# Optimization experiments

Measured on AMD Instinct MI355X. Metric: run time of the kernel, lower is better.

Reference implementation:

```python
import jax, jax.numpy as jnp
import numpy as np

C = 19          # EEG channels
NP = C * C      # 361 channel pairs
D = 256         # UNIFIED_FEATURE_DIM
H = 8           # num_heads
HD = D // H     # head dim


def _build_mask():
    # rel[p, q] = True iff key-pair q shares a channel with query-pair p
    idx = np.arange(NP)
    ci, cj = idx // C, idx % C
    rel = ((ci[:, None] == ci[None, :]) | (ci[:, None] == cj[None, :]) |
           (cj[:, None] == ci[None, :]) | (cj[:, None] == cj[None, :]))
    return jnp.asarray(rel.reshape(C, C, NP))  # (channel_i, j, key_pair)

MASK = _build_mask()


def setup_inputs() -> dict:
    key = jax.random.key(0)
    ks = jax.random.split(key, 6)
    s = 0.05
    return {
        "x": jax.random.normal(ks[0], (32, NP, D), jnp.float32),
        # 19 stacked nn.MultiheadAttention modules: in_proj (3D, D) = [Wq; Wk; Wv]
        "w_in": jax.random.normal(ks[1], (C, 3 * D, D), jnp.float32) * s,
        "b_in": jnp.zeros((C, 3 * D), jnp.float32),
        "w_out": jax.random.normal(ks[2], (C, D, D), jnp.float32) * s,
        "b_out": jnp.zeros((C, D), jnp.float32),
        # fusion: nn.Linear(D, D)
        "w_fuse": jax.random.normal(ks[3], (D, D), jnp.float32) * s,
        "b_fuse": jnp.zeros((D,), jnp.float32),
    }


def reference(x, w_in, b_in, w_out, b_out, w_fuse, b_fuse):
    # x: (B, 361, D). Pair p=(i,j) at index i*19+j uses attention module i,
    # query = x[:, p], keys/values = pairs sharing channel i or j (mask).
    B = x.shape[0]
    wq, wk, wv = w_in[:, :D], w_in[:, D:2 * D], w_in[:, 2 * D:]
    bq, bk, bv = b_in[:, :D], b_in[:, D:2 * D], b_in[:, 2 * D:]

    # Per-channel K/V projections over all 361 pairs: (C, B, NP, D)
    K = jnp.einsum('bnd,ced->cbne', x, wk) + bk[:, None, None, :]
    V = jnp.einsum('bnd,ced->cbne', x, wv) + bv[:, None, None, :]
    # Queries grouped by first channel i: x reshaped to (B, C, C, D)
    xq = x.reshape(B, C, C, D)
    Q = jnp.einsum('bcjd,ced->cbje', xq, wq) + bq[:, None, None, :]  # (C,B,C,D)

    Qh = Q.reshape(C, B, C, H, HD)
    Kh = K.reshape(C, B, NP, H, HD)
    Vh = V.reshape(C, B, NP, H, HD)

    scale = 1.0 / jnp.sqrt(jnp.asarray(HD, x.dtype))
    scores = jnp.einsum('cbqhe,cbkhe->cbhqk', Qh, Kh) * scale  # (C,B,H,C,NP)
    scores = jnp.where(MASK[:, None, None, :, :], scores, -jnp.inf)
    attn = jax.nn.softmax(scores, axis=-1)

    out = jnp.einsum('cbhqk,cbkhe->cbqhe', attn, Vh).reshape(C, B, C, D)
    out = jnp.einsum('cbqd,ced->cbqe', out, w_out) + b_out[:, None, None, :]
    out = out.transpose(1, 0, 2, 3).reshape(B, NP, D)  # back to (B, 361, D)

    # fusion ('linear') + residual
    return out @ w_fuse.T + b_fuse + x
```

## Files before the change

kernel.cpp:

```cpp
#include <hip/hip_runtime.h>

#define CC 19
#define NPOS 361
#define NPAD 384
#define DIM 256
#define TKEY 32
#define NTILES 12

#define LDS_BYTES 69632

using bf16x8 = __attribute__((ext_vector_type(8))) short;
using f16x4  = __attribute__((ext_vector_type(4))) _Float16;
using floatx4 = __attribute__((ext_vector_type(4))) float;
using uintx2 = __attribute__((ext_vector_type(2))) unsigned int;

__device__ __forceinline__ unsigned short f2bf(float f) {
  unsigned u = __builtin_bit_cast(unsigned, f);
  u += 0x7fffu + ((u >> 16) & 1u);
  return (unsigned short)(u >> 16);
}

__device__ __forceinline__ f16x4 pack4h(float a, float b, float c2, float d) {
  const auto h01 = __builtin_amdgcn_cvt_pkrtz(a, b);
  const auto h23 = __builtin_amdgcn_cvt_pkrtz(c2, d);
  uintx2 uv = {__builtin_bit_cast(unsigned, h01), __builtin_bit_cast(unsigned, h23)};
  return __builtin_bit_cast(f16x4, uv);
}

__global__ void conv_all_kernel(const float* __restrict__ x,
                                const float* __restrict__ w_in,
                                const float* __restrict__ w_out,
                                const float* __restrict__ w_fuse,
                                unsigned short* __restrict__ ws) {
  const int j = blockIdx.x * 256 + threadIdx.x;
  float4 v = make_float4(0.f, 0.f, 0.f, 0.f);
  unsigned short* dst;
  if (j < 786432) {
    const int row = j >> 6;
    const int off = (j & 63) << 2;
    const int b = row / NPAD;
    const int r = row - b * NPAD;
    if (r < NPOS) v = *(const float4*)&x[(b * NPOS + r) * DIM + off];
    dst = &ws[row * DIM + off];
  } else if (j < 1720320) {
    const int k = j - 786432;
    v = *(const float4*)&w_in[k << 2];
    dst = &ws[3145728 + (k << 2)];
  } else if (j < 2031616) {
    const int k = j - 1720320;
    v = *(const float4*)&w_out[k << 2];
    dst = &ws[6881280 + (k << 2)];
  } else {
    const int k = j - 2031616;
    v = *(const float4*)&w_fuse[k << 2];
    dst = &ws[8126464 + (k << 2)];
  }
  ushort4 o;
  o.x = f2bf(v.x); o.y = f2bf(v.y); o.z = f2bf(v.z); o.w = f2bf(v.w);
  *(ushort4*)dst = o;
}

__launch_bounds__(256, 2)
__global__ void attn_kernel(const float* __restrict__ b_in,
                            const unsigned short* __restrict__ xbf,
                            const unsigned short* __restrict__ wibf,
                            float* __restrict__ out) {
  const int bid = blockIdx.x;
  const int xcd = bid & 7;
  const int slot = bid >> 3;
  const int c = slot >> 3;
  const int p = ((slot & 7) << 3) | xcd;
  const int b = p >> 1;
  const int hb = p & 1;

  const int tid = threadIdx.x;
  const int w = tid >> 6;
  const int lane = tid & 63;
  const int quad = lane >> 4;
  const int l16 = lane & 15;
  const int eh = (hb * 4 + w) * 32;

  extern __shared__ char smem[];
  unsigned short* sx = (unsigned short*)smem;
  unsigned* msk = (unsigned*)(smem + 67584);
  float* sL = (float*)(smem + 69120);

  const float scale = 0.25503486f;
  const floatx4 fzero = {0.f, 0.f, 0.f, 0.f};

  f16x4 qf[2][2];
  {
    bf16x8 wq[2][8];
#pragma unroll
    for (int m4 = 0; m4 < 2; ++m4)
#pragma unroll
      for (int k = 0; k < 8; ++k)
        wq[m4][k] = *(const bf16x8*)&wibf[(c * 768 + eh + m4 * 16 + l16) * DIM + k * 32 + quad * 8];
    float bq[2][4];
#pragma unroll
    for (int m4 = 0; m4 < 2; ++m4) {
      const float4 bv4 = *(const float4*)&b_in[c * 768 + eh + m4 * 16 + quad * 4];
      bq[m4][0] = bv4.x; bq[m4][1] = bv4.y; bq[m4][2] = bv4.z; bq[m4][3] = bv4.w;
    }
#pragma unroll
    for (int mt = 0; mt < 2; ++mt) {
      const int xrow = b * NPAD + c * CC + mt * 16 + l16;
      bf16x8 xq[8];
#pragma unroll
      for (int k = 0; k < 8; ++k)
        xq[k] = *(const bf16x8*)&xbf[xrow * DIM + k * 32 + quad * 8];
#pragma unroll
      for (int m4 = 0; m4 < 2; ++m4) {
        floatx4 acc = fzero;
#pragma unroll
        for (int k = 0; k < 8; ++k)
          acc = __builtin_amdgcn_mfma_f32_16x16x32_bf16(wq[m4][k], xq[k], acc, 0, 0, 0);
        qf[mt][m4] = pack4h((acc[0] + bq[m4][0]) * scale, (acc[1] + bq[m4][1]) * scale,
                            (acc[2] + bq[m4][2]) * scale, (acc[3] + bq[m4][3]) * scale);
      }
    }
  }

  bf16x8 wk[2][8], wv[2][8];
#pragma unroll
  for (int m4 = 0; m4 < 2; ++m4)
#pragma unroll
    for (int k = 0; k < 8; ++k) {
      wk[m4][k] =
          *(const bf16x8*)&wibf[(c * 768 + 256 + eh + m4 * 16 + l16) * DIM + k * 32 + quad * 8];
      wv[m4][k] =
          *(const bf16x8*)&wibf[(c * 768 + 512 + eh + m4 * 16 + l16) * DIM + k * 32 + quad * 8];
    }
  float bV[2];
#pragma unroll
  for (int ne = 0; ne < 2; ++ne) bV[ne] = b_in[c * 768 + 512 + eh + ne * 16 + l16];

  for (int e2 = tid; e2 < 384; e2 += 256) {
    const int q = e2 / 12;
    const int wd = e2 - q * 12;
    unsigned m = 0u;
    for (int i = 0; i < 32; ++i) {
      const int kabs = wd * 32 + i;
      const unsigned ki = ((unsigned)kabs * 110377u) >> 21;
      const unsigned kj = (unsigned)kabs - ki * 19u;
      if (kabs < NPOS && (ki == (unsigned)c || kj == (unsigned)c ||
                          ki == (unsigned)q || kj == (unsigned)q))
        m |= (1u << i);
    }
    msk[e2] = m;
  }

#pragma unroll
  for (int u = 0; u < 2; ++u)
#pragma unroll
    for (int it = 0; it < 4; ++it) {
      const int cc2 = tid + it * 256;
      const int row = cc2 >> 5;
      const int col = (cc2 & 31) * 8;
      *(bf16x8*)&sx[u * 8448 + row * 264 + col] =
          *(const bf16x8*)&xbf[(b * NPAD + u * TKEY + row) * DIM + col];
    }

  floatx4 o_acc[2][2];
  float lsum[2] = {0.f, 0.f};
#pragma unroll
  for (int mt = 0; mt < 2; ++mt)
#pragma unroll
    for (int ne = 0; ne < 2; ++ne) o_acc[mt][ne] = fzero;

  __syncthreads();

  for (int s6 = 0; s6 < 6; ++s6) {
    const int tb = s6 * 2;
    if (s6 < 5) {
#pragma unroll
      for (int u = 0; u < 2; ++u) {
        const int t = tb + 2 + u;
        unsigned short* bxn = sx + (t & 3) * 8448;
#pragma unroll
        for (int it = 0; it < 4; ++it) {
          const int cc2 = tid + it * 256;
          const int row = cc2 >> 5;
          const int col = (cc2 & 31) * 8;
          *(bf16x8*)&bxn[row * 264 + col] =
              *(const bf16x8*)&xbf[(b * NPAD + t * TKEY + row) * DIM + col];
        }
      }
    }

#pragma unroll
    for (int u = 0; u < 2; ++u) {
      const int t = tb + u;
      const unsigned short* bx = sx + (t & 3) * 8448;

      floatx4 aK[2][2], aV[2][2];
#pragma unroll
      for (int i = 0; i < 2; ++i)
#pragma unroll
        for (int j = 0; j < 2; ++j) { aK[i][j] = fzero; aV[i][j] = fzero; }
#pragma unroll
      for (int k = 0; k < 8; ++k) {
        bf16x8 xfr[2];
#pragma unroll
        for (int n4 = 0; n4 < 2; ++n4)
          xfr[n4] = *(const bf16x8*)&bx[(n4 * 16 + l16) * 264 + k * 32 + quad * 8];
#pragma unroll
        for (int m4 = 0; m4 < 2; ++m4)
#pragma unroll
          for (int n4 = 0; n4 < 2; ++n4) {
            aK[m4][n4] = __builtin_amdgcn_mfma_f32_16x16x32_bf16(wk[m4][k], xfr[n4], aK[m4][n4], 0, 0, 0);
            aV[n4][m4] = __builtin_amdgcn_mfma_f32_16x16x32_bf16(xfr[n4], wv[m4][k], aV[n4][m4], 0, 0, 0);
          }
      }

      f16x4 kf[2][2];
      f16x4 vf[2][2];
#pragma unroll
      for (int kt = 0; kt < 2; ++kt)
#pragma unroll
        for (int ec = 0; ec < 2; ++ec) {
          kf[kt][ec] = pack4h(aK[ec][kt][0], aK[ec][kt][1], aK[ec][kt][2], aK[ec][kt][3]);
          vf[kt][ec] = pack4h(aV[kt][ec][0], aV[kt][ec][1], aV[kt][ec][2], aV[kt][ec][3]);
        }

#pragma unroll
      for (int mt = 0; mt < 2; ++mt) {
        const int q = mt * 16 + l16;
        const unsigned mw = msk[q * 12 + t];
        f16x4 pf[2];
#pragma unroll
        for (int kt = 0; kt < 2; ++kt) {
          floatx4 s2 = __builtin_amdgcn_mfma_f32_16x16x16f16(kf[kt][0], qf[mt][0], fzero, 0, 0, 0);
          s2 = __builtin_amdgcn_mfma_f32_16x16x16f16(kf[kt][1], qf[mt][1], s2, 0, 0, 0);
          const unsigned mk = mw >> (kt * 16 + quad * 4);
          float p[4];
#pragma unroll
          for (int r = 0; r < 4; ++r)
            p[r] = (mk & (1u << r)) ? __builtin_exp2f(s2[r]) : 0.f;
          lsum[mt] += (p[0] + p[1]) + (p[2] + p[3]);
          pf[kt] = pack4h(p[0], p[1], p[2], p[3]);
        }
#pragma unroll
        for (int kt = 0; kt < 2; ++kt)
#pragma unroll
          for (int ne = 0; ne < 2; ++ne)
            o_acc[mt][ne] =
                __builtin_amdgcn_mfma_f32_16x16x16f16(pf[kt], vf[kt][ne], o_acc[mt][ne], 0, 0, 0);
      }
    }
    if (s6 < 5) __syncthreads();
  }

#pragma unroll
  for (int mt = 0; mt < 2; ++mt) {
    lsum[mt] += __shfl_xor(lsum[mt], 16);
    lsum[mt] += __shfl_xor(lsum[mt], 32);
  }
  if (lane < 16) {
    sL[w * 32 + lane] = lsum[0];
    sL[w * 32 + 16 + lane] = lsum[1];
  }
  float invl[2][4];
#pragma unroll
  for (int mt = 0; mt < 2; ++mt)
#pragma unroll
    for (int r = 0; r < 4; ++r)
      invl[mt][r] = 1.f / sL[w * 32 + mt * 16 + quad * 4 + r];

  unsigned short* aop = (unsigned short*)(out + (size_t)(b * NPOS + c * CC) * DIM);
#pragma unroll
  for (int mt = 0; mt < 2; ++mt)
#pragma unroll
    for (int ne = 0; ne < 2; ++ne)
#pragma unroll
      for (int r = 0; r < 4; ++r) {
        const int q = mt * 16 + quad * 4 + r;
        if (q < CC)
          aop[q * DIM + eh + ne * 16 + l16] =
              f2bf(o_acc[mt][ne][r] * invl[mt][r] + bV[ne]);
      }
}

__launch_bounds__(256)
__global__ void epi_kernel(const float* __restrict__ xf,
                           const float* __restrict__ b_out,
                           const float* __restrict__ b_fuse,
                           const unsigned short* __restrict__ wobf,
                           const unsigned short* __restrict__ wfbf,
                           float* __restrict__ out) {
  const int bid = blockIdx.x;
  const int xcd = bid & 7;
  const int slot = bid >> 3;
  const int c = slot >> 2;
  const int b = ((slot & 3) << 3) | xcd;

  const int tid = threadIdx.x;
  const int w = tid >> 6;
  const int lane = tid & 63;
  const int quad = lane >> 4;
  const int l16 = lane & 15;

  __shared__ unsigned short sA[32 * 264];
  __shared__ unsigned short sT[32 * 264];

  const size_t fbase = (size_t)(b * NPOS + c * CC) * DIM;
  const unsigned short* aop = (const unsigned short*)(out + fbase);
  const floatx4 fzero = {0.f, 0.f, 0.f, 0.f};
  const bf16x8 zero8 = {};

#pragma unroll
  for (int it = 0; it < 4; ++it) {
    const int cc2 = tid + it * 256;
    const int row = cc2 >> 5;
    const int col = (cc2 & 31) * 8;
    bf16x8 v = zero8;
    if (row < CC) v = *(const bf16x8*)&aop[row * DIM + col];
    *(bf16x8*)&sA[row * 264 + col] = v;
  }
  __syncthreads();

#pragma unroll
  for (int mt = 0; mt < 2; ++mt) {
    bf16x8 a8[8];
#pragma unroll
    for (int k = 0; k < 8; ++k)
      a8[k] = *(const bf16x8*)&sA[(mt * 16 + l16) * 264 + k * 32 + quad * 8];
#pragma unroll
    for (int nt2 = 0; nt2 < 4; ++nt2) {
      const int e0 = w * 64 + nt2 * 16;
      floatx4 acc = fzero;
#pragma unroll
      for (int k = 0; k < 8; ++k) {
        bf16x8 b8 = *(const bf16x8*)&wobf[(c * 256 + e0 + l16) * DIM + k * 32 + quad * 8];
        acc = __builtin_amdgcn_mfma_f32_16x16x32_bf16(a8[k], b8, acc, 0, 0, 0);
      }
      const float bias = b_out[c * 256 + e0 + l16];
#pragma unroll
      for (int r = 0; r < 4; ++r)
        sT[(mt * 16 + quad * 4 + r) * 264 + e0 + l16] = f2bf(acc[r] + bias);
    }
  }
  __syncthreads();

#pragma unroll
  for (int mt = 0; mt < 2; ++mt) {
    bf16x8 a8[8];
#pragma unroll
    for (int k = 0; k < 8; ++k)
      a8[k] = *(const bf16x8*)&sT[(mt * 16 + l16) * 264 + k * 32 + quad * 8];
#pragma unroll
    for (int nt2 = 0; nt2 < 4; ++nt2) {
      const int e0 = w * 64 + nt2 * 16;
      floatx4 acc = fzero;
#pragma unroll
      for (int k = 0; k < 8; ++k) {
        bf16x8 b8 = *(const bf16x8*)&wfbf[(e0 + l16) * DIM + k * 32 + quad * 8];
        acc = __builtin_amdgcn_mfma_f32_16x16x32_bf16(a8[k], b8, acc, 0, 0, 0);
      }
      const float bfu = b_fuse[e0 + l16];
#pragma unroll
      for (int r = 0; r < 4; ++r) {
        const int row = mt * 16 + quad * 4 + r;
        if (row < CC) {
          const size_t gp = fbase + (size_t)row * DIM + e0 + l16;
          out[gp] = acc[r] + bfu + xf[gp];
        }
      }
    }
  }
}

extern "C" void kernel_launch(void* const* d_in, const int* in_sizes, int n_in,
                              void* d_out, int out_size, void* d_ws, size_t ws_size,
                              hipStream_t stream) {
  const float* x      = (const float*)d_in[0];
  const float* w_in   = (const float*)d_in[1];
  const float* b_in   = (const float*)d_in[2];
  const float* w_out  = (const float*)d_in[3];
  const float* b_out  = (const float*)d_in[4];
  const float* w_fuse = (const float*)d_in[5];
  const float* b_fuse = (const float*)d_in[6];
  float* out = (float*)d_out;

  if (ws_size < (size_t)16384000) return;

  unsigned short* ws = (unsigned short*)d_ws;
  unsigned short* x_bf  = ws;
  unsigned short* wi_bf = ws + 3145728;
  unsigned short* wo_bf = ws + 6881280;
  unsigned short* wf_bf = ws + 8126464;

  conv_all_kernel<<<8000, 256, 0, stream>>>(x, w_in, w_out, w_fuse, ws);

  (void)hipFuncSetAttribute((const void*)attn_kernel,
                            hipFuncAttributeMaxDynamicSharedMemorySize, LDS_BYTES);
  attn_kernel<<<1216, 256, LDS_BYTES, stream>>>(b_in, x_bf, wi_bf, out);

  epi_kernel<<<608, 256, 0, stream>>>(x, b_out, b_fuse, wo_bf, wf_bf, out);
}
```

Before: 244.4 us.

## Load x tiles directly to LDS with swizzle, add setprio, widen epilogue blocks

The attention kernel now stages x tiles with global_load_lds (direct global-to-LDS DMA) into an unpadded, XOR-swizzled layout instead of register round-trip stores into a padded layout. The aim is to cut VGPR traffic and LDS bank conflicts and to shrink the LDS footprint. MFMA sections are wrapped in s_setprio to favour the matrix phases across waves. The epilogue kernel moves to 512 threads per block, each wave covering half as many output columns. The direct-to-LDS loads are not visibly waited on before the barrier, so correctness depends on how the compiler inserts vmcnt waits.

```diff
diff --git a/kernel.cpp b/kernel.cpp
--- a/kernel.cpp
+++ b/kernel.cpp
@@ -7,7 +7,7 @@
 #define TKEY 32
 #define NTILES 12
 
-#define LDS_BYTES 69632
+#define LDS_BYTES 67584
 
 using bf16x8 = __attribute__((ext_vector_type(8))) short;
 using f16x4  = __attribute__((ext_vector_type(4))) _Float16;
@@ -25,6 +25,12 @@
   const auto h23 = __builtin_amdgcn_cvt_pkrtz(c2, d);
   uintx2 uv = {__builtin_bit_cast(unsigned, h01), __builtin_bit_cast(unsigned, h23)};
   return __builtin_bit_cast(f16x4, uv);
+}
+
+__device__ __forceinline__ void gload_lds16(const void* g, void* l) {
+  __builtin_amdgcn_global_load_lds(
+      (const __attribute__((address_space(1))) void*)g,
+      (__attribute__((address_space(3))) void*)l, 16, 0, 0);
 }
 
 __global__ void conv_all_kernel(const float* __restrict__ x,
@@ -81,12 +87,27 @@
   const int eh = (hb * 4 + w) * 32;
 
   extern __shared__ char smem[];
-  unsigned short* sx = (unsigned short*)smem;
-  unsigned* msk = (unsigned*)(smem + 67584);
-  float* sL = (float*)(smem + 69120);
+  char* sx = smem;
+  unsigned* msk = (unsigned*)(smem + 65536);
+  float* sL = (float*)(smem + 67072);
 
   const float scale = 0.25503486f;
   const floatx4 fzero = {0.f, 0.f, 0.f, 0.f};
+
+  const int xw = (l16 & 7) << 4;
+  const size_t xrowbytes = (size_t)b * NPAD * 512;
+
+#pragma unroll
+  for (int u = 0; u < 2; ++u) {
+#pragma unroll
+    for (int call = 0; call < 4; ++call) {
+      const int sbyte = w * 4096 + call * 1024 + (lane << 4);
+      const int row = sbyte >> 9;
+      const int inner = (sbyte & 511) ^ ((row & 7) << 4);
+      gload_lds16((const char*)xbf + xrowbytes + (size_t)(u * TKEY + row) * 512 + inner,
+                  sx + u * 16384 + w * 4096 + call * 1024);
+    }
+  }
 
   f16x4 qf[2][2];
   {
@@ -150,17 +171,6 @@
     msk[e2] = m;
   }
 
-#pragma unroll
-  for (int u = 0; u < 2; ++u)
-#pragma unroll
-    for (int it = 0; it < 4; ++it) {
-      const int cc2 = tid + it * 256;
-      const int row = cc2 >> 5;
-      const int col = (cc2 & 31) * 8;
-      *(bf16x8*)&sx[u * 8448 + row * 264 + col] =
-          *(const bf16x8*)&xbf[(b * NPAD + u * TKEY + row) * DIM + col];
-    }
-
   floatx4 o_acc[2][2];
   float lsum[2] = {0.f, 0.f};
 #pragma unroll
@@ -176,14 +186,14 @@
 #pragma unroll
       for (int u = 0; u < 2; ++u) {
         const int t = tb + 2 + u;
-        unsigned short* bxn = sx + (t & 3) * 8448;
-#pragma unroll
-        for (int it = 0; it < 4; ++it) {
-          const int cc2 = tid + it * 256;
-          const int row = cc2 >> 5;
-          const int col = (cc2 & 31) * 8;
-          *(bf16x8*)&bxn[row * 264 + col] =
-              *(const bf16x8*)&xbf[(b * NPAD + t * TKEY + row) * DIM + col];
+        char* bxn = sx + (t & 3) * 16384;
+#pragma unroll
+        for (int call = 0; call < 4; ++call) {
+          const int sbyte = w * 4096 + call * 1024 + (lane << 4);
+          const int row = sbyte >> 9;
+          const int inner = (sbyte & 511) ^ ((row & 7) << 4);
+          gload_lds16((const char*)xbf + xrowbytes + (size_t)(t * TKEY + row) * 512 + inner,
+                      bxn + w * 4096 + call * 1024);
         }
       }
     }
@@ -191,19 +201,23 @@
 #pragma unroll
     for (int u = 0; u < 2; ++u) {
       const int t = tb + u;
-      const unsigned short* bx = sx + (t & 3) * 8448;
+      const char* bx = sx + (t & 3) * 16384;
 
       floatx4 aK[2][2], aV[2][2];
 #pragma unroll
       for (int i = 0; i < 2; ++i)
 #pragma unroll
         for (int j = 0; j < 2; ++j) { aK[i][j] = fzero; aV[i][j] = fzero; }
+      __builtin_amdgcn_s_setprio(1);
 #pragma unroll
       for (int k = 0; k < 8; ++k) {
         bf16x8 xfr[2];
 #pragma unroll
-        for (int n4 = 0; n4 < 2; ++n4)
-          xfr[n4] = *(const bf16x8*)&bx[(n4 * 16 + l16) * 264 + k * 32 + quad * 8];
+        for (int n4 = 0; n4 < 2; ++n4) {
+          const int row = n4 * 16 + l16;
+          const int inner = (k * 64 + quad * 16) ^ xw;
+          xfr[n4] = *(const bf16x8*)(bx + row * 512 + inner);
+        }
 #pragma unroll
         for (int m4 = 0; m4 < 2; ++m4)
 #pragma unroll
@@ -212,6 +226,7 @@
             aV[n4][m4] = __builtin_amdgcn_mfma_f32_16x16x32_bf16(xfr[n4], wv[m4][k], aV[n4][m4], 0, 0, 0);
           }
       }
+      __builtin_amdgcn_s_setprio(0);
 
       f16x4 kf[2][2];
       f16x4 vf[2][2];
@@ -240,12 +255,14 @@
           lsum[mt] += (p[0] + p[1]) + (p[2] + p[3]);
           pf[kt] = pack4h(p[0], p[1], p[2], p[3]);
         }
+        __builtin_amdgcn_s_setprio(1);
 #pragma unroll
         for (int kt = 0; kt < 2; ++kt)
 #pragma unroll
           for (int ne = 0; ne < 2; ++ne)
             o_acc[mt][ne] =
                 __builtin_amdgcn_mfma_f32_16x16x16f16(pf[kt], vf[kt][ne], o_acc[mt][ne], 0, 0, 0);
+        __builtin_amdgcn_s_setprio(0);
       }
     }
     if (s6 < 5) __syncthreads();
@@ -281,7 +298,7 @@
       }
 }
 
-__launch_bounds__(256)
+__launch_bounds__(512)
 __global__ void epi_kernel(const float* __restrict__ xf,
                            const float* __restrict__ b_out,
                            const float* __restrict__ b_fuse,
@@ -309,8 +326,8 @@
   const bf16x8 zero8 = {};
 
 #pragma unroll
-  for (int it = 0; it < 4; ++it) {
-    const int cc2 = tid + it * 256;
+  for (int it = 0; it < 2; ++it) {
+    const int cc2 = tid + it * 512;
     const int row = cc2 >> 5;
     const int col = (cc2 & 31) * 8;
     bf16x8 v = zero8;
@@ -326,8 +343,8 @@
     for (int k = 0; k < 8; ++k)
       a8[k] = *(const bf16x8*)&sA[(mt * 16 + l16) * 264 + k * 32 + quad * 8];
 #pragma unroll
-    for (int nt2 = 0; nt2 < 4; ++nt2) {
-      const int e0 = w * 64 + nt2 * 16;
+    for (int nt2 = 0; nt2 < 2; ++nt2) {
+      const int e0 = w * 32 + nt2 * 16;
       floatx4 acc = fzero;
 #pragma unroll
       for (int k = 0; k < 8; ++k) {
@@ -349,8 +366,8 @@
     for (int k = 0; k < 8; ++k)
       a8[k] = *(const bf16x8*)&sT[(mt * 16 + l16) * 264 + k * 32 + quad * 8];
 #pragma unroll
-    for (int nt2 = 0; nt2 < 4; ++nt2) {
-      const int e0 = w * 64 + nt2 * 16;
+    for (int nt2 = 0; nt2 < 2; ++nt2) {
+      const int e0 = w * 32 + nt2 * 16;
       floatx4 acc = fzero;
 #pragma unroll
       for (int k = 0; k < 8; ++k) {
@@ -396,5 +413,5 @@
                             hipFuncAttributeMaxDynamicSharedMemorySize, LDS_BYTES);
   attn_kernel<<<1216, 256, LDS_BYTES, stream>>>(b_in, x_bf, wi_bf, out);
 
-  epi_kernel<<<608, 256, 0, stream>>>(x, b_out, b_fuse, wo_bf, wf_bf, out);
-}
+  epi_kernel<<<608, 512, 0, stream>>>(x, b_out, b_fuse, wo_bf, wf_bf, out);
+}
```

New measurement: 233.5 us (median of 6 runs). 4.5% less time.
